# Kernel optimization log

Measured on AMD Instinct MI355X. Metric: run time of the kernel, lower is better.

## Reference

```python
import jax, jax.numpy as jnp
import numpy as np

EPS = 1e-6

def _ln(x, gamma, beta):
    # torch LayerNorm variant: unbiased std, denominator (std + eps)
    mean = jnp.mean(x, axis=-1, keepdims=True)
    std = jnp.std(x, axis=-1, keepdims=True, ddof=1)
    return gamma * (x - mean) / (std + EPS) + beta

def _hyper_lstm_step(x, h, c, hyper_h, hyper_c,
                     hc_Wih, hc_bih, hc_Whh, hc_ln_gamma, hc_ln_beta,
                     hc_lnc_gamma, hc_lnc_beta,
                     Wph, bph, Wpx, bpx, Wpb, Wsh, Wsx, Wsb,
                     Wih, Whh, bias, ln_gamma, ln_beta, lnc_gamma, lnc_beta):
    B = x.shape[0]
    H = h.shape[1]
    Hh = hyper_h.shape[1]
    # ---- hyper LSTM cell (input = [x, h]) ----
    hyper_in = jnp.concatenate([x, h], axis=1)                      # [B, In+H]
    v = hyper_in @ hc_Wih.T + hc_bih + hyper_h @ hc_Whh.T           # [B, 4*Hh]
    v = v.reshape(B, 4, Hh)
    v = _ln(v, hc_ln_gamma, hc_ln_beta)                             # parallel LN over 4 gates
    hi, hf, hg, ho = v[:, 0], v[:, 1], v[:, 2], v[:, 3]
    hf = hf + 1.0
    new_hyper_c = hyper_c * jax.nn.sigmoid(hf) + jax.nn.sigmoid(hi) * jnp.tanh(hg)
    new_hyper_c = _ln(new_hyper_c, hc_lnc_gamma, hc_lnc_beta)
    new_hyper_h = jnp.tanh(new_hyper_c) * jax.nn.sigmoid(ho)        # [B, Hh]
    # ---- hyper modulation vectors: scale(proj(hyper_h)) for each gate/source ----
    # proj: [B,Hh] x [4,E,Hh] -> [B,4,E]; scale: [B,4,E] x [4,H,E] -> [B,4,H]
    zh = jnp.einsum('bge,ghe->bgh', jnp.einsum('bk,gek->bge', new_hyper_h, Wph) + bph, Wsh)
    zx = jnp.einsum('bge,ghe->bgh', jnp.einsum('bk,gek->bge', new_hyper_h, Wpx) + bpx, Wsx)
    zb = jnp.einsum('bge,ghe->bgh', jnp.einsum('bk,gek->bge', new_hyper_h, Wpb), Wsb)
    # ---- main LSTM gates ----
    xh = (x @ Wih.T).reshape(B, 4, H)
    hh = (h @ Whh.T).reshape(B, 4, H)
    gates = xh * zx + hh * zh + (bias.reshape(4, H) + zb)           # [B,4,H]
    # f gets +1 before layer norm (as in source)
    gates = gates + jnp.array([0.0, 1.0, 0.0, 0.0], gates.dtype)[None, :, None]
    gates = _ln(gates, ln_gamma, ln_beta)
    i, f, g, o = gates[:, 0], gates[:, 1], gates[:, 2], gates[:, 3]
    new_c = c * jax.nn.sigmoid(f) + jax.nn.sigmoid(i) * jnp.tanh(g)  # dropout is identity (eval)
    new_c = _ln(new_c, lnc_gamma, lnc_beta)
    new_h = jnp.tanh(new_c) * jax.nn.sigmoid(o)
    return new_h, new_c, new_hyper_h, new_hyper_c

def setup_inputs() -> dict:
    key = jax.random.key(0)
    B, In, H, Hh, E = 512, 2048, 2048, 256, 64
    ks = jax.random.split(key, 16)
    s = 0.02
    return {
        'x': jax.random.normal(ks[0], (B, In), jnp.float32),
        'h': jax.random.normal(ks[1], (B, H), jnp.float32),
        'c': jax.random.normal(ks[2], (B, H), jnp.float32),
        'hyper_h': jax.random.normal(ks[3], (B, Hh), jnp.float32),
        'hyper_c': jax.random.normal(ks[4], (B, Hh), jnp.float32),
        'hc_Wih': jax.random.normal(ks[5], (4 * Hh, In + H), jnp.float32) * s,
        'hc_bih': jnp.zeros((4 * Hh,), jnp.float32),
        'hc_Whh': jax.random.normal(ks[6], (4 * Hh, Hh), jnp.float32) * s,
        'hc_ln_gamma': jnp.ones((4, Hh), jnp.float32),
        'hc_ln_beta': jnp.zeros((4, Hh), jnp.float32),
        'hc_lnc_gamma': jnp.ones((Hh,), jnp.float32),
        'hc_lnc_beta': jnp.zeros((Hh,), jnp.float32),
        'Wph': jax.random.normal(ks[7], (4, E, Hh), jnp.float32) * s,
        'bph': jnp.ones((4, E), jnp.float32),
        'Wpx': jax.random.normal(ks[8], (4, E, Hh), jnp.float32) * s,
        'bpx': jnp.ones((4, E), jnp.float32),
        'Wpb': jax.random.normal(ks[9], (4, E, Hh), jnp.float32) * 0.01,
        'Wsh': jnp.full((4, H, E), 0.1 / E, jnp.float32),
        'Wsx': jnp.full((4, H, E), 0.1 / E, jnp.float32),
        'Wsb': jax.random.normal(ks[10], (4, H, E), jnp.float32) * s,
        'Wih': jax.random.normal(ks[11], (4 * H, In), jnp.float32) * s,
        'Whh': jax.random.normal(ks[12], (4 * H, H), jnp.float32) * s,
        'bias': jnp.zeros((4 * H,), jnp.float32),
        'ln_gamma': jnp.ones((4, H), jnp.float32),
        'ln_beta': jnp.zeros((4, H), jnp.float32),
        'lnc_gamma': jnp.ones((H,), jnp.float32),
        'lnc_beta': jnp.zeros((H,), jnp.float32),
    }

def reference(x, h, c, hyper_h, hyper_c, hc_Wih, hc_bih, hc_Whh, hc_ln_gamma,
              hc_ln_beta, hc_lnc_gamma, hc_lnc_beta, Wph, bph, Wpx, bpx, Wpb,
              Wsh, Wsx, Wsb, Wih, Whh, bias, ln_gamma, ln_beta, lnc_gamma, lnc_beta):
    return _hyper_lstm_step(x, h, c, hyper_h, hyper_c, hc_Wih, hc_bih, hc_Whh,
                            hc_ln_gamma, hc_ln_beta, hc_lnc_gamma, hc_lnc_beta,
                            Wph, bph, Wpx, bpx, Wpb, Wsh, Wsx, Wsb,
                            Wih, Whh, bias, ln_gamma, ln_beta, lnc_gamma, lnc_beta)
```

## Files before the change

### kernel.cpp

```cpp
#include <hip/hip_runtime.h>
#include <hip/hip_bf16.h>
#include <math.h>

typedef __attribute__((ext_vector_type(4))) float  f32x4;
typedef __attribute__((ext_vector_type(8))) __bf16 bf16x8;

#define LN_EPS 1e-6f

__device__ __forceinline__ float sigf(float v){ return 1.f / (1.f + __expf(-v)); }
__device__ __forceinline__ float tanh_f(float v){
  float t = __expf(-2.f * fabsf(v));
  float r = (1.f - t) / (1.f + t);
  return copysignf(r, v);
}
__device__ __forceinline__ float wave_sum(float v){
  #pragma unroll
  for(int m = 1; m < 64; m <<= 1) v += __shfl_xor(v, m, 64);
  return v;
}

__device__ __forceinline__ unsigned short f2bf(float f){
  return __builtin_bit_cast(unsigned short, static_cast<__bf16>(f));
}
__device__ __forceinline__ unsigned int pk_bf16(float a, float b){
  return (unsigned int)f2bf(a) | ((unsigned int)f2bf(b) << 16);
}
__device__ __forceinline__ float bfu(unsigned int u){
  unsigned int t = u << 16;
  return __builtin_bit_cast(float, t);
}

template<int NROWS, int NTHR>
__device__ __forceinline__ void stage_tile(const float* __restrict__ src, int row_stride,
                                           unsigned short* lds, int tid){
  constexpr int PER = (NROWS * 16) / NTHR;
  #pragma unroll
  for(int s = 0; s < PER; ++s){
    int fi  = tid + s * NTHR;
    int row = fi >> 4, kf = fi & 15;
    float4 v = *(reinterpret_cast<const float4*>(src + row * row_stride) + kf);
    unsigned int lo = pk_bf16(v.x, v.y), hi = pk_bf16(v.z, v.w);
    int byte = ((row << 7) + (kf << 3)) ^ ((row & 7) << 4);
    uint2 u; u.x = lo; u.y = hi;
    *reinterpret_cast<uint2*>(reinterpret_cast<char*>(lds) + byte) = u;
  }
}

template<int NROWS>
struct Stage {
  float4 v[(NROWS * 16) / 256];
  __device__ __forceinline__ void load(const float* __restrict__ src, int stride, int tid){
    #pragma unroll
    for(int s = 0; s < (NROWS * 16) / 256; ++s){
      int fi = tid + s * 256;
      v[s] = *(reinterpret_cast<const float4*>(src + (fi >> 4) * stride) + (fi & 15));
    }
  }
  __device__ __forceinline__ void write(unsigned short* lds, int tid){
    #pragma unroll
    for(int s = 0; s < (NROWS * 16) / 256; ++s){
      int fi = tid + s * 256;
      int row = fi >> 4, kf = fi & 15;
      unsigned int lo = pk_bf16(v[s].x, v[s].y), hi = pk_bf16(v[s].z, v[s].w);
      int byte = ((row << 7) + (kf << 3)) ^ ((row & 7) << 4);
      uint2 u; u.x = lo; u.y = hi;
      *reinterpret_cast<uint2*>(reinterpret_cast<char*>(lds) + byte) = u;
    }
  }
};

__device__ __forceinline__ bf16x8 read_frag(const unsigned short* lds, int row, int ks, int lane){
  int byte = ((row << 7) + ((ks + ((lane >> 4) << 3)) << 1)) ^ ((row & 7) << 4);
  return *reinterpret_cast<const bf16x8*>(reinterpret_cast<const char*>(lds) + byte);
}

__global__ __launch_bounds__(256, 2) void k1_hyper_gemm(
    const float* __restrict__ x, const float* __restrict__ h,
    const float* __restrict__ hyper_h, const float* __restrict__ hc_Wih,
    const float* __restrict__ hc_Whh,
    unsigned short* __restrict__ v1, unsigned short* __restrict__ v2){
  __shared__ unsigned short Ab[32 * 64];
  __shared__ unsigned short Bb[32 * 64];
  int tid = threadIdx.x, lane = tid & 63, w = tid >> 6;
  int wr = w >> 1, wc = w & 1;
  int fid = blockIdx.x;
  int half = fid >> 9, rid = fid & 511;
  int n0 = (rid & 31) * 32, m0 = (rid >> 5) * 32;
  unsigned short* vo = half ? v2 : v1;
  int kb = half * 2176;
  f32x4 acc = {0.f, 0.f, 0.f, 0.f};

  #pragma unroll 1
  for(int kk = 0; kk < 2176; kk += 64){
    int k0 = kb + kk;
    const float* as; int ast;
    if(k0 < 2048)      { as = x       + m0 * 2048 + k0;          ast = 2048; }
    else if(k0 < 4096) { as = h       + m0 * 2048 + (k0 - 2048); ast = 2048; }
    else               { as = hyper_h + m0 * 256  + (k0 - 4096); ast = 256;  }
    const float* bs; int bst;
    if(k0 < 4096)      { bs = hc_Wih  + n0 * 4096 + k0;          bst = 4096; }
    else               { bs = hc_Whh  + n0 * 256  + (k0 - 4096); bst = 256;  }
    __syncthreads();
    stage_tile<32, 256>(as, ast, Ab, tid);
    stage_tile<32, 256>(bs, bst, Bb, tid);
    __syncthreads();
    #pragma unroll
    for(int ks = 0; ks < 64; ks += 32){
      bf16x8 af = read_frag(Ab, wr * 16 + (lane & 15), ks, lane);
      bf16x8 bf = read_frag(Bb, wc * 16 + (lane & 15), ks, lane);
      acc = __builtin_amdgcn_mfma_f32_16x16x32_bf16(af, bf, acc, 0, 0, 0);
    }
  }
  int n = n0 + wc * 16 + (lane & 15);
  #pragma unroll
  for(int r = 0; r < 4; ++r){
    int m = m0 + wr * 16 + (lane >> 4) * 4 + r;
    vo[m * 1024 + n] = f2bf(acc[r]);
  }
}

__global__ __launch_bounds__(256) void k2_hyper_cell(
    const unsigned short* __restrict__ v1, const unsigned short* __restrict__ v2,
    const float* __restrict__ bih, const float* __restrict__ hyper_c,
    const float* __restrict__ lng, const float* __restrict__ lnb,
    const float* __restrict__ lncg, const float* __restrict__ lncb,
    float* __restrict__ out){
  int tid = threadIdx.x, lane = tid & 63, w = tid >> 6;
  int b = blockIdx.x * 4 + w;
  float vn[4][4];
  #pragma unroll
  for(int g = 0; g < 4; ++g){
    float vv[4], s = 0.f;
    #pragma unroll
    for(int q = 0; q < 4; ++q){
      int e = lane + 64 * q;
      int bi = b * 1024 + g * 256 + e;
      vv[q] = bfu(v1[bi]) + bfu(v2[bi]) + bih[g * 256 + e];
      s += vv[q];
    }
    float mean = wave_sum(s) * (1.f / 256.f);
    float sse = 0.f;
    #pragma unroll
    for(int q = 0; q < 4; ++q){ float d = vv[q] - mean; sse += d * d; }
    float inv = 1.f / (sqrtf(wave_sum(sse) * (1.f / 255.f)) + LN_EPS);
    #pragma unroll
    for(int q = 0; q < 4; ++q){
      int e = lane + 64 * q;
      vn[g][q] = lng[g * 256 + e] * (vv[q] - mean) * inv + lnb[g * 256 + e];
    }
  }
  float ncr[4], os[4], s2 = 0.f;
  #pragma unroll
  for(int q = 0; q < 4; ++q){
    float hc = hyper_c[b * 256 + lane + 64 * q];
    float hi = vn[0][q], hf = vn[1][q] + 1.f, hg = vn[2][q], ho = vn[3][q];
    ncr[q] = hc * sigf(hf) + sigf(hi) * tanh_f(hg);
    os[q]  = sigf(ho);
    s2 += ncr[q];
  }
  float mean2 = wave_sum(s2) * (1.f / 256.f);
  float sse2 = 0.f;
  #pragma unroll
  for(int q = 0; q < 4; ++q){ float d = ncr[q] - mean2; sse2 += d * d; }
  float inv2 = 1.f / (sqrtf(wave_sum(sse2) * (1.f / 255.f)) + LN_EPS);
  #pragma unroll
  for(int q = 0; q < 4; ++q){
    int e = lane + 64 * q;
    float ncn = lncg[e] * (ncr[q] - mean2) * inv2 + lncb[e];
    out[2097152 + b * 256 + e] = tanh_f(ncn) * os[q];
    out[2228224 + b * 256 + e] = ncn;
  }
}

__global__ __launch_bounds__(256, 2) void k3_pmat(
    const float* __restrict__ nhh, const float* __restrict__ Wph,
    const float* __restrict__ Wpx, const float* __restrict__ Wpb,
    const float* __restrict__ bph, const float* __restrict__ bpx,
    float* __restrict__ P){
  __shared__ unsigned short Ab[64 * 64];
  __shared__ unsigned short Bb[64 * 64];
  int tid = threadIdx.x, lane = tid & 63, w = tid >> 6;
  int wr = w >> 1, wc = w & 1;
  int n0 = blockIdx.x * 64, m0 = blockIdx.y * 64;
  int j3 = n0 >> 8, jr0 = n0 & 255;
  const float* W = (j3 == 0) ? Wph : (j3 == 1) ? Wpx : Wpb;
  f32x4 acc[2][2];
  const f32x4 zf = {0.f, 0.f, 0.f, 0.f};
  #pragma unroll
  for(int i = 0; i < 2; ++i){ acc[i][0] = zf; acc[i][1] = zf; }

  #pragma unroll 1
  for(int k0 = 0; k0 < 256; k0 += 64){
    __syncthreads();
    stage_tile<64, 256>(nhh + m0 * 256 + k0, 256, Ab, tid);
    stage_tile<64, 256>(W + jr0 * 256 + k0, 256, Bb, tid);
    __syncthreads();
    #pragma unroll
    for(int ks = 0; ks < 64; ks += 32){
      bf16x8 af[2], bfr[2];
      #pragma unroll
      for(int i = 0; i < 2; ++i) af[i]  = read_frag(Ab, wr * 32 + i * 16 + (lane & 15), ks, lane);
      #pragma unroll
      for(int j = 0; j < 2; ++j) bfr[j] = read_frag(Bb, wc * 32 + j * 16 + (lane & 15), ks, lane);
      #pragma unroll
      for(int i = 0; i < 2; ++i){
        #pragma unroll
        for(int j = 0; j < 2; ++j)
          acc[i][j] = __builtin_amdgcn_mfma_f32_16x16x32_bf16(af[i], bfr[j], acc[i][j], 0, 0, 0);
      }
    }
  }
  #pragma unroll
  for(int j = 0; j < 2; ++j){
    int cj = jr0 + wc * 32 + j * 16 + (lane & 15);
    float bv = (j3 == 0) ? bph[cj] : (j3 == 1) ? bpx[cj] : 0.f;
    int n = n0 + wc * 32 + j * 16 + (lane & 15);
    #pragma unroll
    for(int i = 0; i < 2; ++i){
      #pragma unroll
      for(int r = 0; r < 4; ++r){
        int m = m0 + wr * 32 + i * 16 + (lane >> 4) * 4 + r;
        P[m * 768 + n] = acc[i][j][r] + bv;
      }
    }
  }
}

__global__ __launch_bounds__(256, 2) void k4_gates(
    const float* __restrict__ x, const float* __restrict__ h,
    const float* __restrict__ Wih, const float* __restrict__ Whh,
    const float* __restrict__ bias, const float* __restrict__ P,
    const float* __restrict__ Wsh, const float* __restrict__ Wsx,
    const float* __restrict__ Wsb,
    unsigned short* __restrict__ g1, unsigned short* __restrict__ g2){
  __shared__ unsigned short Ab[2][64 * 64];
  __shared__ unsigned short Bb[2][128 * 64];
  int tid = threadIdx.x, lane = tid & 63, w = tid >> 6;
  int wr = w >> 1, wc = w & 1;
  int fid = blockIdx.x;
  int role = fid >> 9;
  int rid = fid & 511;
  int xcd = rid & 7, idx = rid >> 3;
  int nt = xcd * 8 + (idx >> 3);
  int mt = idx & 7;
  int n0 = nt << 7, m0 = mt << 6;
  int g = n0 >> 11, hc0 = n0 & 2047;

  const float* V  = role ? h : x;
  const float* W  = role ? Whh : Wih;
  const float* Pm = P + m0 * 768 + (role ? 0 : 256) + g * 64;
  const float* Ws = (role ? Wsh : Wsx) + (g * 2048 + hc0) * 64;

  f32x4 accZ[2][4], accW[2][4];
  Stage<64>  LA;
  Stage<128> LB;

  auto zero = [&](f32x4 (&a)[2][4]){
    const f32x4 zf = {0.f, 0.f, 0.f, 0.f};
    #pragma unroll
    for(int i = 0; i < 2; ++i)
      #pragma unroll
      for(int j = 0; j < 4; ++j) a[i][j] = zf;
  };
  auto mfma_on = [&](const unsigned short* A_, const unsigned short* B_, f32x4 (&acc)[2][4]){
    #pragma unroll
    for(int ks = 0; ks < 64; ks += 32){
      bf16x8 af[2], bfr[4];
      #pragma unroll
      for(int i = 0; i < 2; ++i) af[i]  = read_frag(A_, wr * 32 + i * 16 + (lane & 15), ks, lane);
      #pragma unroll
      for(int j = 0; j < 4; ++j) bfr[j] = read_frag(B_, wc * 64 + j * 16 + (lane & 15), ks, lane);
      #pragma unroll
      for(int i = 0; i < 2; ++i){
        #pragma unroll
        for(int j = 0; j < 4; ++j)
          acc[i][j] = __builtin_amdgcn_mfma_f32_16x16x32_bf16(af[i], bfr[j], acc[i][j], 0, 0, 0);
      }
    }
  };

  zero(accZ); zero(accW);

  stage_tile<64, 256>(Pm, 768, Ab[0], tid);
  stage_tile<128, 256>(Ws, 64, Bb[0], tid);
  LA.load(V + m0 * 2048, 2048, tid);
  LB.load(W + n0 * 2048, 2048, tid);
  __syncthreads();
  mfma_on(Ab[0], Bb[0], accZ);
  __syncthreads();
  LA.write(Ab[0], tid); LB.write(Bb[0], tid);
  LA.load(V + m0 * 2048 + 64, 2048, tid);
  LB.load(W + n0 * 2048 + 64, 2048, tid);
  __syncthreads();

  #pragma unroll 1
  for(int t = 0; t < 32; ++t){
    if(t + 1 < 32){
      LA.write(Ab[(t + 1) & 1], tid);
      LB.write(Bb[(t + 1) & 1], tid);
      if(t + 2 < 32){
        LA.load(V + m0 * 2048 + (t + 2) * 64, 2048, tid);
        LB.load(W + n0 * 2048 + (t + 2) * 64, 2048, tid);
      }
    }
    mfma_on(Ab[t & 1], Bb[t & 1], accW);
    __syncthreads();
  }

  if(role == 0){
    #pragma unroll
    for(int j = 0; j < 4; ++j){
      int n = n0 + wc * 64 + j * 16 + (lane & 15);
      #pragma unroll
      for(int i = 0; i < 2; ++i){
        #pragma unroll
        for(int r = 0; r < 4; ++r){
          int m = m0 + wr * 32 + i * 16 + (lane >> 4) * 4 + r;
          g1[m * 8192 + n] = f2bf(accW[i][j][r] * accZ[i][j][r]);
        }
      }
    }
  } else {
    #pragma unroll
    for(int i = 0; i < 2; ++i)
      #pragma unroll
      for(int j = 0; j < 4; ++j)
        #pragma unroll
        for(int r = 0; r < 4; ++r)
          accW[i][j][r] *= accZ[i][j][r];
    zero(accZ);
    stage_tile<64, 256>(P + m0 * 768 + 512 + g * 64, 768, Ab[0], tid);
    stage_tile<128, 256>(Wsb + (g * 2048 + hc0) * 64, 64, Bb[0], tid);
    __syncthreads();
    mfma_on(Ab[0], Bb[0], accZ);
    #pragma unroll
    for(int j = 0; j < 4; ++j){
      int n = n0 + wc * 64 + j * 16 + (lane & 15);
      float bv = bias[n];
      #pragma unroll
      for(int i = 0; i < 2; ++i){
        #pragma unroll
        for(int r = 0; r < 4; ++r){
          int m = m0 + wr * 32 + i * 16 + (lane >> 4) * 4 + r;
          g2[m * 8192 + n] = f2bf(accW[i][j][r] + accZ[i][j][r] + bv);
        }
      }
    }
  }
}

__global__ __launch_bounds__(256) void k5_cell(
    const unsigned short* __restrict__ g1, const unsigned short* __restrict__ g2,
    const float* __restrict__ c,
    const float* __restrict__ lng, const float* __restrict__ lnb,
    const float* __restrict__ lncg, const float* __restrict__ lncb,
    float* __restrict__ out){
  __shared__ float G[4 * 2048];
  __shared__ float red[4];
  int tid = threadIdx.x, lane = tid & 63, w = tid >> 6;
  int b = blockIdx.x;
  const unsigned short* r1 = g1 + b * 8192 + w * 2048 + lane * 32;
  const unsigned short* r2 = g2 + b * 8192 + w * 2048 + lane * 32;
  float gv[32]; float s = 0.f;
  #pragma unroll
  for(int t = 0; t < 4; ++t){
    uint4 a  = *reinterpret_cast<const uint4*>(r1 + t * 8);
    uint4 bb = *reinterpret_cast<const uint4*>(r2 + t * 8);
    unsigned int aw[4] = {a.x, a.y, a.z, a.w};
    unsigned int bw[4] = {bb.x, bb.y, bb.z, bb.w};
    #pragma unroll
    for(int k = 0; k < 4; ++k){
      float f0 = bfu(aw[k] & 0xffffu) + bfu(bw[k] & 0xffffu);
      float f1 = bfu(aw[k] >> 16)     + bfu(bw[k] >> 16);
      gv[t * 8 + 2 * k]     = f0;
      gv[t * 8 + 2 * k + 1] = f1;
      s += f0 + f1;
    }
  }
  float mean = wave_sum(s) * (1.f / 2048.f);
  float sse = 0.f;
  #pragma unroll
  for(int q = 0; q < 32; ++q){ float d = gv[q] - mean; sse += d * d; }
  float inv = 1.f / (sqrtf(wave_sum(sse) * (1.f / 2047.f)) + LN_EPS);
  #pragma unroll
  for(int q = 0; q < 32; ++q){
    int e = w * 2048 + lane * 32 + q;
    G[e] = lng[e] * (gv[q] - mean) * inv + lnb[e];
  }
  __syncthreads();
  float nc[8], os[8], s2 = 0.f;
  #pragma unroll
  for(int q = 0; q < 8; ++q){
    int e = tid + 256 * q;
    float iv = G[e], fv = G[2048 + e], gg = G[4096 + e], ov = G[6144 + e];
    float cc = c[b * 2048 + e];
    nc[q] = cc * sigf(fv) + sigf(iv) * tanh_f(gg);
    os[q] = sigf(ov);
    s2 += nc[q];
  }
  s2 = wave_sum(s2);
  if(lane == 0) red[w] = s2;
  __syncthreads();
  float mean2 = (red[0] + red[1] + red[2] + red[3]) * (1.f / 2048.f);
  float sse2 = 0.f;
  #pragma unroll
  for(int q = 0; q < 8; ++q){ float d = nc[q] - mean2; sse2 += d * d; }
  sse2 = wave_sum(sse2);
  __syncthreads();
  if(lane == 0) red[w] = sse2;
  __syncthreads();
  float inv2 = 1.f / (sqrtf((red[0] + red[1] + red[2] + red[3]) * (1.f / 2047.f)) + LN_EPS);
  #pragma unroll
  for(int q = 0; q < 8; ++q){
    int e = tid + 256 * q;
    float ncn = lncg[e] * (nc[q] - mean2) * inv2 + lncb[e];
    out[b * 2048 + e]           = tanh_f(ncn) * os[q];
    out[1048576 + b * 2048 + e] = ncn;
  }
}

extern "C" void kernel_launch(void* const* d_in, const int* in_sizes, int n_in,
                              void* d_out, int out_size, void* d_ws, size_t ws_size,
                              hipStream_t stream){
  const float* x        = (const float*)d_in[0];
  const float* h        = (const float*)d_in[1];
  const float* c        = (const float*)d_in[2];
  const float* hyper_h  = (const float*)d_in[3];
  const float* hyper_c  = (const float*)d_in[4];
  const float* hc_Wih   = (const float*)d_in[5];
  const float* hc_bih   = (const float*)d_in[6];
  const float* hc_Whh   = (const float*)d_in[7];
  const float* hc_lng   = (const float*)d_in[8];
  const float* hc_lnb   = (const float*)d_in[9];
  const float* hc_lncg  = (const float*)d_in[10];
  const float* hc_lncb  = (const float*)d_in[11];
  const float* Wph      = (const float*)d_in[12];
  const float* bph      = (const float*)d_in[13];
  const float* Wpx      = (const float*)d_in[14];
  const float* bpx      = (const float*)d_in[15];
  const float* Wpb      = (const float*)d_in[16];
  const float* Wsh      = (const float*)d_in[17];
  const float* Wsx      = (const float*)d_in[18];
  const float* Wsb      = (const float*)d_in[19];
  const float* Wih      = (const float*)d_in[20];
  const float* Whh      = (const float*)d_in[21];
  const float* bias     = (const float*)d_in[22];
  const float* ln_g     = (const float*)d_in[23];
  const float* ln_b     = (const float*)d_in[24];
  const float* lnc_g    = (const float*)d_in[25];
  const float* lnc_b    = (const float*)d_in[26];

  float* out = (float*)d_out;
  unsigned short* ws_v1 = (unsigned short*)d_ws;
  unsigned short* ws_v2 = ws_v1 + 524288;
  float*          ws_P  = (float*)(ws_v2 + 524288);
  unsigned short* ws_g1 = (unsigned short*)(ws_P + 393216);
  unsigned short* ws_g2 = ws_g1 + 4194304;
  const float* nhh = out + 2097152;

  k1_hyper_gemm<<<1024, 256, 0, stream>>>(x, h, hyper_h, hc_Wih, hc_Whh, ws_v1, ws_v2);
  k2_hyper_cell<<<128, 256, 0, stream>>>(ws_v1, ws_v2, hc_bih, hyper_c, hc_lng, hc_lnb, hc_lncg, hc_lncb, out);
  k3_pmat<<<dim3(12, 8), 256, 0, stream>>>(nhh, Wph, Wpx, Wpb, bph, bpx, ws_P);
  k4_gates<<<1024, 256, 0, stream>>>(x, h, Wih, Whh, bias, ws_P, Wsh, Wsx, Wsb, ws_g1, ws_g2);
  k5_cell<<<512, 256, 0, stream>>>(ws_g1, ws_g2, c, ln_g, ln_b, lnc_g, lnc_b, out);
}
```

Baseline: 131.6 us.

## Pre-convert gate weights to bf16 and stage them with direct global-to-LDS loads

Adds a conversion kernel that writes Wih, Whh, x and h as bf16 into workspace on every call. When the workspace is large enough, a new gates kernel loads tiles straight into LDS with global_load_lds instead of staging fp32 values through registers. This trades an extra full pass over the large weight matrices (fp32 read plus bf16 write) for halved bytes and simpler staging in the GEMM. The new GEMM uses a single LDS buffer with two barriers per k-step, so loads no longer overlap compute, and it falls back to the old kernel if the workspace is too small.

```diff
diff --git a/kernel.cpp b/kernel.cpp
--- a/kernel.cpp
+++ b/kernel.cpp
@@ -47,31 +47,47 @@
 }
 
 template<int NROWS>
-struct Stage {
-  float4 v[(NROWS * 16) / 256];
-  __device__ __forceinline__ void load(const float* __restrict__ src, int stride, int tid){
-    #pragma unroll
-    for(int s = 0; s < (NROWS * 16) / 256; ++s){
-      int fi = tid + s * 256;
-      v[s] = *(reinterpret_cast<const float4*>(src + (fi >> 4) * stride) + (fi & 15));
-    }
-  }
-  __device__ __forceinline__ void write(unsigned short* lds, int tid){
-    #pragma unroll
-    for(int s = 0; s < (NROWS * 16) / 256; ++s){
-      int fi = tid + s * 256;
-      int row = fi >> 4, kf = fi & 15;
-      unsigned int lo = pk_bf16(v[s].x, v[s].y), hi = pk_bf16(v[s].z, v[s].w);
-      int byte = ((row << 7) + (kf << 3)) ^ ((row & 7) << 4);
-      uint2 u; u.x = lo; u.y = hi;
-      *reinterpret_cast<uint2*>(reinterpret_cast<char*>(lds) + byte) = u;
-    }
-  }
-};
+__device__ __forceinline__ void dma_tile(const unsigned short* __restrict__ src,
+                                         int row_stride_elems,
+                                         unsigned short* lds, int tid){
+  constexpr int PER = (NROWS * 8) / 256;
+  #pragma unroll
+  for(int s = 0; s < PER; ++s){
+    int G   = tid + s * 256;
+    int r   = G >> 3;
+    int kf2 = (G & 7) ^ (r & 7);
+    const char* gp = reinterpret_cast<const char*>(src + r * row_stride_elems) + kf2 * 16;
+    char* lp = reinterpret_cast<char*>(lds) + ((tid & ~63) + s * 256) * 16;
+    __builtin_amdgcn_global_load_lds(
+        (const __attribute__((address_space(1))) unsigned int*)gp,
+        (__attribute__((address_space(3))) unsigned int*)lp, 16, 0, 0);
+  }
+}
 
 __device__ __forceinline__ bf16x8 read_frag(const unsigned short* lds, int row, int ks, int lane){
   int byte = ((row << 7) + ((ks + ((lane >> 4) << 3)) << 1)) ^ ((row & 7) << 4);
   return *reinterpret_cast<const bf16x8*>(reinterpret_cast<const char*>(lds) + byte);
+}
+
+__global__ __launch_bounds__(256) void kconv(
+    const float* __restrict__ Wih, const float* __restrict__ Whh,
+    const float* __restrict__ x, const float* __restrict__ h,
+    unsigned short* __restrict__ dst){
+  const long nW = 16777216 / 4, nX = 1048576 / 4;
+  const long total = 2 * nW + 2 * nX;
+  long i = (long)blockIdx.x * 256 + threadIdx.x;
+  long stride = (long)gridDim.x * 256;
+  for(; i < total; i += stride){
+    const float* src; long off;
+    if(i < nW)            { src = Wih; off = i; }
+    else if(i < 2*nW)     { src = Whh; off = i - nW; }
+    else if(i < 2*nW+nX)  { src = x;   off = i - 2*nW; }
+    else                  { src = h;   off = i - 2*nW - nX; }
+    float4 v = reinterpret_cast<const float4*>(src)[off];
+    ushort4 o;
+    o.x = f2bf(v.x); o.y = f2bf(v.y); o.z = f2bf(v.z); o.w = f2bf(v.w);
+    reinterpret_cast<ushort4*>(dst)[i] = o;
+  }
 }
 
 __global__ __launch_bounds__(256, 2) void k1_hyper_gemm(
@@ -226,7 +242,138 @@
   }
 }
 
-__global__ __launch_bounds__(256, 2) void k4_gates(
+__global__ __launch_bounds__(256, 2) void k4_gates_dma(
+    const unsigned short* __restrict__ xbf, const unsigned short* __restrict__ hbf,
+    const unsigned short* __restrict__ Wihbf, const unsigned short* __restrict__ Whhbf,
+    const float* __restrict__ bias, const float* __restrict__ P,
+    const float* __restrict__ Wsh, const float* __restrict__ Wsx,
+    const float* __restrict__ Wsb,
+    unsigned short* __restrict__ g1, unsigned short* __restrict__ g2){
+  __shared__ unsigned short Ab[64 * 64];
+  __shared__ unsigned short Bb[128 * 64];
+  int tid = threadIdx.x, lane = tid & 63, w = tid >> 6;
+  int wr = w >> 1, wc = w & 1;
+  int fid = blockIdx.x;
+  int role = fid >> 9;
+  int rid = fid & 511;
+  int xcd = rid & 7, idx = rid >> 3;
+  int nt = xcd * 8 + (idx >> 3);
+  int mt = idx & 7;
+  int n0 = nt << 7, m0 = mt << 6;
+  int g = n0 >> 11, hc0 = n0 & 2047;
+
+  const unsigned short* V = role ? hbf : xbf;
+  const unsigned short* W = role ? Whhbf : Wihbf;
+  const float* Pm = P + m0 * 768 + (role ? 0 : 256) + g * 64;
+  const float* Ws = (role ? Wsh : Wsx) + (g * 2048 + hc0) * 64;
+
+  f32x4 accZ[2][4], accW[2][4];
+  auto zero = [&](f32x4 (&a)[2][4]){
+    const f32x4 zf = {0.f, 0.f, 0.f, 0.f};
+    #pragma unroll
+    for(int i = 0; i < 2; ++i)
+      #pragma unroll
+      for(int j = 0; j < 4; ++j) a[i][j] = zf;
+  };
+  auto mfma_on = [&](f32x4 (&acc)[2][4]){
+    #pragma unroll
+    for(int ks = 0; ks < 64; ks += 32){
+      bf16x8 af[2], bfr[4];
+      #pragma unroll
+      for(int i = 0; i < 2; ++i) af[i]  = read_frag(Ab, wr * 32 + i * 16 + (lane & 15), ks, lane);
+      #pragma unroll
+      for(int j = 0; j < 4; ++j) bfr[j] = read_frag(Bb, wc * 64 + j * 16 + (lane & 15), ks, lane);
+      #pragma unroll
+      for(int i = 0; i < 2; ++i){
+        #pragma unroll
+        for(int j = 0; j < 4; ++j)
+          acc[i][j] = __builtin_amdgcn_mfma_f32_16x16x32_bf16(af[i], bfr[j], acc[i][j], 0, 0, 0);
+      }
+    }
+  };
+
+  zero(accZ); zero(accW);
+  stage_tile<64, 256>(Pm, 768, Ab, tid);
+  stage_tile<128, 256>(Ws, 64, Bb, tid);
+  __syncthreads();
+  mfma_on(accZ);
+
+  #pragma unroll 1
+  for(int t = 0; t < 32; ++t){
+    __syncthreads();
+    dma_tile<64>(V + m0 * 2048 + t * 64, 2048, Ab, tid);
+    dma_tile<128>(W + n0 * 2048 + t * 64, 2048, Bb, tid);
+    __syncthreads();
+    mfma_on(accW);
+  }
+
+  if(role == 0){
+    #pragma unroll
+    for(int j = 0; j < 4; ++j){
+      int n = n0 + wc * 64 + j * 16 + (lane & 15);
+      #pragma unroll
+      for(int i = 0; i < 2; ++i){
+        #pragma unroll
+        for(int r = 0; r < 4; ++r){
+          int m = m0 + wr * 32 + i * 16 + (lane >> 4) * 4 + r;
+          g1[m * 8192 + n] = f2bf(accW[i][j][r] * accZ[i][j][r]);
+        }
+      }
+    }
+  } else {
+    #pragma unroll
+    for(int i = 0; i < 2; ++i)
+      #pragma unroll
+      for(int j = 0; j < 4; ++j)
+        #pragma unroll
+        for(int r = 0; r < 4; ++r)
+          accW[i][j][r] *= accZ[i][j][r];
+    zero(accZ);
+    __syncthreads();
+    stage_tile<64, 256>(P + m0 * 768 + 512 + g * 64, 768, Ab, tid);
+    stage_tile<128, 256>(Wsb + (g * 2048 + hc0) * 64, 64, Bb, tid);
+    __syncthreads();
+    mfma_on(accZ);
+    #pragma unroll
+    for(int j = 0; j < 4; ++j){
+      int n = n0 + wc * 64 + j * 16 + (lane & 15);
+      float bv = bias[n];
+      #pragma unroll
+      for(int i = 0; i < 2; ++i){
+        #pragma unroll
+        for(int r = 0; r < 4; ++r){
+          int m = m0 + wr * 32 + i * 16 + (lane >> 4) * 4 + r;
+          g2[m * 8192 + n] = f2bf(accW[i][j][r] + accZ[i][j][r] + bv);
+        }
+      }
+    }
+  }
+}
+
+template<int NROWS>
+struct Stage {
+  float4 v[(NROWS * 16) / 256];
+  __device__ __forceinline__ void load(const float* __restrict__ src, int stride, int tid){
+    #pragma unroll
+    for(int s = 0; s < (NROWS * 16) / 256; ++s){
+      int fi = tid + s * 256;
+      v[s] = *(reinterpret_cast<const float4*>(src + (fi >> 4) * stride) + (fi & 15));
+    }
+  }
+  __device__ __forceinline__ void write(unsigned short* lds, int tid){
+    #pragma unroll
+    for(int s = 0; s < (NROWS * 16) / 256; ++s){
+      int fi = tid + s * 256;
+      int row = fi >> 4, kf = fi & 15;
+      unsigned int lo = pk_bf16(v[s].x, v[s].y), hi = pk_bf16(v[s].z, v[s].w);
+      int byte = ((row << 7) + (kf << 3)) ^ ((row & 7) << 4);
+      uint2 u; u.x = lo; u.y = hi;
+      *reinterpret_cast<uint2*>(reinterpret_cast<char*>(lds) + byte) = u;
+    }
+  }
+};
+
+__global__ __launch_bounds__(256, 2) void k4_gates_reg(
     const float* __restrict__ x, const float* __restrict__ h,
     const float* __restrict__ Wih, const float* __restrict__ Whh,
     const float* __restrict__ bias, const float* __restrict__ P,
@@ -280,7 +427,6 @@
   };
 
   zero(accZ); zero(accW);
-
   stage_tile<64, 256>(Pm, 768, Ab[0], tid);
   stage_tile<128, 256>(Ws, 64, Bb[0], tid);
   LA.load(V + m0 * 2048, 2048, tid);
@@ -456,11 +602,24 @@
   float*          ws_P  = (float*)(ws_v2 + 524288);
   unsigned short* ws_g1 = (unsigned short*)(ws_P + 393216);
   unsigned short* ws_g2 = ws_g1 + 4194304;
+  unsigned short* ws_bf = ws_g2 + 4194304;
+  unsigned short* Wihbf = ws_bf;
+  unsigned short* Whhbf = Wihbf + 16777216;
+  unsigned short* xbf   = Whhbf + 16777216;
+  unsigned short* hbf   = xbf + 1048576;
+  const size_t WS_NEED = 91750400;
   const float* nhh = out + 2097152;
 
+  bool dma = (ws_size >= WS_NEED);
+
+  if(dma)
+    kconv<<<2048, 256, 0, stream>>>(Wih, Whh, x, h, ws_bf);
   k1_hyper_gemm<<<1024, 256, 0, stream>>>(x, h, hyper_h, hc_Wih, hc_Whh, ws_v1, ws_v2);
   k2_hyper_cell<<<128, 256, 0, stream>>>(ws_v1, ws_v2, hc_bih, hyper_c, hc_lng, hc_lnb, hc_lncg, hc_lncb, out);
   k3_pmat<<<dim3(12, 8), 256, 0, stream>>>(nhh, Wph, Wpx, Wpb, bph, bpx, ws_P);
-  k4_gates<<<1024, 256, 0, stream>>>(x, h, Wih, Whh, bias, ws_P, Wsh, Wsx, Wsb, ws_g1, ws_g2);
+  if(dma)
+    k4_gates_dma<<<1024, 256, 0, stream>>>(xbf, hbf, Wihbf, Whhbf, bias, ws_P, Wsh, Wsx, Wsb, ws_g1, ws_g2);
+  else
+    k4_gates_reg<<<1024, 256, 0, stream>>>(x, h, Wih, Whh, bias, ws_P, Wsh, Wsx, Wsb, ws_g1, ws_g2);
   k5_cell<<<512, 256, 0, stream>>>(ws_g1, ws_g2, c, ln_g, ln_b, lnc_g, lnc_b, out);
 }
```

Result: slower. 154.2 us (+17.2%).
